# Optimization experiments

Measured on AMD Instinct MI355X. Metric: run time of the kernel, lower is better.

## Reference

```python
import jax, jax.numpy as jnp
import numpy as np

B, N, D, H = 1, 512, 128, 128  # batch, seq, pair dim, hidden dim
EPS = 1e-6  # flax nnx LayerNorm default epsilon


def _layernorm(x, scale, bias):
    m = jnp.mean(x, axis=-1, keepdims=True)
    v = jnp.var(x, axis=-1, keepdims=True)
    return (x - m) * jax.lax.rsqrt(v + EPS) * scale + bias


def setup_inputs() -> dict:
    key = jax.random.key(0)
    ks = jax.random.split(key, 12)
    s = 0.02  # param init scale
    inp = {
        "x": jax.random.normal(ks[0], (B, N, N, D), jnp.float32),
        "src_mask": jnp.ones((B, N), jnp.float32),
        # first LayerNorm
        "ln1_scale": jnp.ones((D,), jnp.float32),
        "ln1_bias": jnp.zeros((D,), jnp.float32),
        # left/right projections
        "wl": jax.random.normal(ks[1], (D, H), jnp.float32) * s,
        "bl": jnp.zeros((H,), jnp.float32),
        "wr": jax.random.normal(ks[2], (D, H), jnp.float32) * s,
        "br": jnp.zeros((H,), jnp.float32),
        # gates (original inits kernel=0, bias=1; use small random kernels + bias=1 for a nontrivial baseline)
        "wlg": jax.random.normal(ks[3], (D, H), jnp.float32) * s,
        "blg": jnp.ones((H,), jnp.float32),
        "wrg": jax.random.normal(ks[4], (D, H), jnp.float32) * s,
        "brg": jnp.ones((H,), jnp.float32),
        "wog": jax.random.normal(ks[5], (D, H), jnp.float32) * s,
        "bog": jnp.ones((H,), jnp.float32),
        # output LayerNorm + projection
        "ln2_scale": jnp.ones((H,), jnp.float32),
        "ln2_bias": jnp.zeros((H,), jnp.float32),
        "wo": jax.random.normal(ks[6], (H, D), jnp.float32) * s,
        "bo": jnp.zeros((D,), jnp.float32),
    }
    return inp


def reference(x, src_mask, ln1_scale, ln1_bias, wl, bl, wr, br, wlg, blg,
              wrg, brg, wog, bog, ln2_scale, ln2_bias, wo, bo):
    # mask[b,i,j] = src_mask[b,i] * src_mask[b,j]  -> [B,N,N,1]
    sm = src_mask.astype(jnp.float32)
    mask = (sm[:, :, None] * sm[:, None, :])[..., None]

    xn = _layernorm(x, ln1_scale, ln1_bias)  # [B,N,N,D]

    # projections, mask, gates (gating after transpose in the original is
    # elementwise, hence equivalent applied pre-transpose)
    left = (xn @ wl + bl) * mask * jax.nn.sigmoid(xn @ wlg + blg)   # [B,N,N,H]
    right = (xn @ wr + br) * mask * jax.nn.sigmoid(xn @ wrg + brg)  # [B,N,N,H]
    out_gate = jax.nn.sigmoid(xn @ wog + bog)                       # [B,N,N,H]

    # 'ingoing' mix: out[b,i,j,d] = sum_k left[b,k,i,d] * right[b,k,j,d]
    out = jnp.einsum('bkid,bkjd->bijd', left, right)

    out = _layernorm(out, ln2_scale, ln2_bias) * out_gate
    return out @ wo + bo
```

## Files before the change

### kernel.cpp

```cpp
#include <hip/hip_runtime.h>
#include <hip/hip_bf16.h>


#define NSEQ 512
#define NN 262144
#define DMODEL 128

typedef __attribute__((ext_vector_type(8))) short short8;
typedef __attribute__((ext_vector_type(4))) float f32x4;

__device__ __forceinline__ unsigned short f2b(float f) {
    __hip_bfloat16 h = __float2bfloat16(f);
    return *reinterpret_cast<unsigned short*>(&h);
}
__device__ __forceinline__ float b2f(unsigned short u) {
    __hip_bfloat16 h;
    *reinterpret_cast<unsigned short*>(&h) = u;
    return __bfloat162float(h);
}
__device__ __forceinline__ float sigmoidf_(float x) {
    return 1.0f / (1.0f + __expf(-x));
}

__global__ __launch_bounds__(256) void k_wt_all(
    const float* __restrict__ w0, const float* __restrict__ w1,
    const float* __restrict__ w2, const float* __restrict__ w3,
    const float* __restrict__ w4, const float* __restrict__ w5,
    unsigned short* __restrict__ wt) {
    int bid = blockIdx.x;
    int mat = bid >> 6;
    const float* w = (mat == 0) ? w0 : (mat == 1) ? w1 : (mat == 2) ? w2
                   : (mat == 3) ? w3 : (mat == 4) ? w4 : w5;
    int idx = (bid & 63) * 256 + threadIdx.x;
    int d = idx >> 7, h = idx & 127;
    wt[mat * 16384 + h * 128 + d] = f2b(w[idx]);
}

__global__ __launch_bounds__(256) void k_ln1(const float* __restrict__ x,
                                             const float* __restrict__ sc,
                                             const float* __restrict__ bi,
                                             unsigned short* __restrict__ xn) {
    int t = threadIdx.x;
    int l = t & 31;
    size_t row = (size_t)blockIdx.x * 8 + (t >> 5);
    float4 v = *(const float4*)(x + row * DMODEL + l * 4);
    float s  = v.x + v.y + v.z + v.w;
    float sq = v.x * v.x + v.y * v.y + v.z * v.z + v.w * v.w;
    #pragma unroll
    for (int m = 1; m < 32; m <<= 1) {
        s  += __shfl_xor(s, m);
        sq += __shfl_xor(sq, m);
    }
    float mean = s * (1.f / 128.f);
    float var  = sq * (1.f / 128.f) - mean * mean;
    float inv  = rsqrtf(var + 1e-6f);
    float4 scv = *(const float4*)(sc + l * 4);
    float4 biv = *(const float4*)(bi + l * 4);
    unsigned long long o = 0;
    o |= (unsigned long long)f2b((v.x - mean) * inv * scv.x + biv.x);
    o |= (unsigned long long)f2b((v.y - mean) * inv * scv.y + biv.y) << 16;
    o |= (unsigned long long)f2b((v.z - mean) * inv * scv.z + biv.z) << 32;
    o |= (unsigned long long)f2b((v.w - mean) * inv * scv.w + biv.w) << 48;
    *(unsigned long long*)(xn + row * DMODEL + l * 4) = o;
}

__global__ __launch_bounds__(256, 2) void k_proj(
    const unsigned short* __restrict__ xn,
    const float* __restrict__ src_mask,
    const unsigned short* __restrict__ wt,
    const float* __restrict__ bl,  const float* __restrict__ blg,
    const float* __restrict__ br,  const float* __restrict__ brg,
    const float* __restrict__ bog,
    unsigned short* __restrict__ left_t,
    unsigned short* __restrict__ right_t,
    unsigned short* __restrict__ og) {
    __shared__ __align__(16) unsigned short As[64 * 136];
    const int t = threadIdx.x;
    const int lane = t & 63;
    const int wv = t >> 6;
    const int a0 = blockIdx.x * 64;
    const int b  = blockIdx.y;
    const int n0 = wv * 32;

    short8 bfA[2][4], bfB[2][4];
    auto loadB = [&](short8 (&dst)[2][4], int mat) {
        const unsigned short* base = wt + mat * 16384 + (lane >> 4) * 8;
        #pragma unroll
        for (int nf = 0; nf < 2; ++nf)
            #pragma unroll
            for (int kc = 0; kc < 4; ++kc)
                dst[nf][kc] = *(const short8*)(
                    base + (n0 + nf * 16 + (lane & 15)) * 128 + kc * 32);
    };
    loadB(bfA, 0);
    loadB(bfB, 1);

    #pragma unroll
    for (int it = 0; it < 4; ++it) {
        int idx = it * 256 + t;
        int row = idx >> 4, c = idx & 15;
        *(short8*)(&As[row * 136 + c * 8]) =
            *(const short8*)(xn + ((size_t)(a0 + row) * NSEQ + b) * DMODEL + c * 8);
    }
    __syncthreads();

    short8 af[4][4];
    #pragma unroll
    for (int mf = 0; mf < 4; ++mf)
        #pragma unroll
        for (int kc = 0; kc < 4; ++kc)
            af[mf][kc] = *(const short8*)(
                &As[(mf * 16 + (lane & 15)) * 136 + kc * 32 + (lane >> 4) * 8]);

    f32x4 acc0[4][2], acc1[4][2];
    float smb = src_mask[b];

    auto mmat = [&](f32x4 (&acc)[4][2], short8 (&bf)[2][4]) {
        #pragma unroll
        for (int mf = 0; mf < 4; ++mf)
            #pragma unroll
            for (int nf = 0; nf < 2; ++nf)
                acc[mf][nf] = f32x4{0.f, 0.f, 0.f, 0.f};
        #pragma unroll
        for (int kc = 0; kc < 4; ++kc)
            #pragma unroll
            for (int mf = 0; mf < 4; ++mf)
                #pragma unroll
                for (int nf = 0; nf < 2; ++nf)
                    acc[mf][nf] = __builtin_amdgcn_mfma_f32_16x16x32_bf16(
                        af[mf][kc], bf[nf][kc], acc[mf][nf], 0, 0, 0);
    };
    auto epi_pair = [&](const float* b1, const float* b2, unsigned short* dst) {
        #pragma unroll
        for (int nf = 0; nf < 2; ++nf) {
            int h = n0 + nf * 16 + (lane & 15);
            float b1v = b1[h], b2v = b2[h];
            #pragma unroll
            for (int mf = 0; mf < 4; ++mf) {
                int abase = a0 + mf * 16 + ((lane >> 4) << 2);
                unsigned long long pv64 = 0;
                #pragma unroll
                for (int j = 0; j < 4; ++j) {
                    float pv = acc0[mf][nf][j] + b1v;
                    float gv = acc1[mf][nf][j] + b2v;
                    float mk = src_mask[abase + j] * smb;
                    unsigned long long q = f2b(pv * mk * sigmoidf_(gv));
                    pv64 |= q << (16 * j);
                }
                *(unsigned long long*)(dst + (size_t)h * NN + (size_t)b * NSEQ + abase) = pv64;
            }
        }
    };

    mmat(acc0, bfA);
    loadB(bfA, 2);
    mmat(acc1, bfB);
    loadB(bfB, 3);
    epi_pair(bl, blg, left_t);
    mmat(acc0, bfA);
    loadB(bfA, 4);
    mmat(acc1, bfB);
    epi_pair(br, brg, right_t);
    mmat(acc0, bfA);

    __syncthreads();
    #pragma unroll
    for (int nf = 0; nf < 2; ++nf) {
        int h = n0 + nf * 16 + (lane & 15);
        float bv = bog[h];
        #pragma unroll
        for (int mf = 0; mf < 4; ++mf) {
            int rloc = mf * 16 + ((lane >> 4) << 2);
            #pragma unroll
            for (int j = 0; j < 4; ++j)
                As[(rloc + j) * 136 + h] = f2b(sigmoidf_(acc0[mf][nf][j] + bv));
        }
    }
    __syncthreads();
    #pragma unroll
    for (int it = 0; it < 4; ++it) {
        int idx = it * 256 + t;
        int row = idx >> 4, c = idx & 15;
        *(short8*)(og + ((size_t)(a0 + row) * NSEQ + b) * DMODEL + c * 8) =
            *(const short8*)(&As[row * 136 + c * 8]);
    }
}

__global__ __launch_bounds__(256) void k_einsum(
    const unsigned short* __restrict__ lt,
    const unsigned short* __restrict__ rt,
    unsigned short* __restrict__ mid) {
    __shared__ __align__(16) unsigned short As[2][128 * 36];
    __shared__ __align__(16) unsigned short Bs[2][128 * 36];
    const int t = threadIdx.x, lane = t & 63, wv = t >> 6;
    const int bid = blockIdx.x;
    const int xcd = bid & 7, slot = bid >> 3;
    const int d = xcd * 16 + (slot >> 4);
    const int tile = slot & 15;
    const int i0 = (tile >> 2) * 128, j0 = (tile & 3) * 128;
    const int m0 = (wv >> 1) * 64, n0 = (wv & 1) * 64;
    const unsigned short* Ag = lt + (size_t)d * NN;
    const unsigned short* Bg = rt + (size_t)d * NN;

    const int row0 = t >> 2, sub0 = t & 3;
    const int row1 = (256 + t) >> 2, sub1 = t & 3;

    short8 ra[2], rb[2];
    auto loadTile = [&](int k0) {
        ra[0] = *(const short8*)(Ag + (size_t)(i0 + row0) * NSEQ + k0 + sub0 * 8);
        rb[0] = *(const short8*)(Bg + (size_t)(j0 + row0) * NSEQ + k0 + sub0 * 8);
        ra[1] = *(const short8*)(Ag + (size_t)(i0 + row1) * NSEQ + k0 + sub1 * 8);
        rb[1] = *(const short8*)(Bg + (size_t)(j0 + row1) * NSEQ + k0 + sub1 * 8);
    };
    auto writeTile = [&](int buf) {
        *(short8*)(&As[buf][row0 * 36 + sub0 * 8]) = ra[0];
        *(short8*)(&Bs[buf][row0 * 36 + sub0 * 8]) = rb[0];
        *(short8*)(&As[buf][row1 * 36 + sub1 * 8]) = ra[1];
        *(short8*)(&Bs[buf][row1 * 36 + sub1 * 8]) = rb[1];
    };

    f32x4 acc[4][4];
    #pragma unroll
    for (int mf = 0; mf < 4; ++mf)
        #pragma unroll
        for (int nf = 0; nf < 4; ++nf)
            acc[mf][nf] = f32x4{0.f, 0.f, 0.f, 0.f};

    loadTile(0);
    writeTile(0);
    int cur = 0;
    const int ko = (lane >> 4) * 8;
    for (int it = 0; it < 16; ++it) {
        __syncthreads();
        if (it < 15) loadTile((it + 1) * 32);
        short8 af[4], bf[4];
        #pragma unroll
        for (int mf = 0; mf < 4; ++mf)
            af[mf] = *(const short8*)(&As[cur][(m0 + mf * 16 + (lane & 15)) * 36 + ko]);
        #pragma unroll
        for (int nf = 0; nf < 4; ++nf)
            bf[nf] = *(const short8*)(&Bs[cur][(n0 + nf * 16 + (lane & 15)) * 36 + ko]);
        #pragma unroll
        for (int mf = 0; mf < 4; ++mf)
            #pragma unroll
            for (int nf = 0; nf < 4; ++nf)
                acc[mf][nf] = __builtin_amdgcn_mfma_f32_16x16x32_bf16(
                    af[mf], bf[nf], acc[mf][nf], 0, 0, 0);
        if (it < 15) writeTile(cur ^ 1);
        cur ^= 1;
    }
    unsigned short* out = mid + (size_t)d * NN;
    #pragma unroll
    for (int mf = 0; mf < 4; ++mf) {
        int rbase = i0 + m0 + mf * 16 + ((lane >> 4) << 2);
        #pragma unroll
        for (int nf = 0; nf < 4; ++nf) {
            int col = j0 + n0 + nf * 16 + (lane & 15);
            #pragma unroll
            for (int j = 0; j < 4; ++j)
                out[(size_t)(rbase + j) * NSEQ + col] = f2b(acc[mf][nf][j]);
        }
    }
}

__global__ __launch_bounds__(128) void k_ln2gate(
    const unsigned short* __restrict__ mid,
    const unsigned short* __restrict__ og,
    const float* __restrict__ sc, const float* __restrict__ bi,
    unsigned short* __restrict__ g) {
    __shared__ __align__(16) unsigned short lo[128 * 136];
    const int t = threadIdx.x;
    const size_t p0 = (size_t)blockIdx.x * 128;
    const size_t p = p0 + t;

    unsigned int vals[64];
    float s = 0.f, sq = 0.f;
    #pragma unroll
    for (int d2 = 0; d2 < 64; ++d2) {
        unsigned int a = mid[(size_t)(2 * d2)     * NN + p];
        unsigned int c = mid[(size_t)(2 * d2 + 1) * NN + p];
        vals[d2] = a | (c << 16);
        float fa = b2f((unsigned short)a), fc = b2f((unsigned short)c);
        s += fa + fc; sq += fa * fa + fc * fc;
    }
    float mean = s * (1.f / 128.f);
    float var  = sq * (1.f / 128.f) - mean * mean;
    float inv  = rsqrtf(var + 1e-6f);
    #pragma unroll
    for (int c = 0; c < 16; ++c) {
        short8 ov = *(const short8*)(og + p * DMODEL + c * 8);
        short8 r8;
        #pragma unroll
        for (int e = 0; e < 8; ++e) {
            int d = c * 8 + e;
            unsigned int w = vals[d >> 1];
            float v = b2f((unsigned short)((d & 1) ? (w >> 16) : (w & 0xffff)));
            float y = (v - mean) * inv * sc[d] + bi[d];
            r8[e] = (short)f2b(y * b2f((unsigned short)ov[e]));
        }
        *(short8*)(&lo[t * 136 + c * 8]) = r8;
    }
    __syncthreads();
    #pragma unroll
    for (int i = 0; i < 16; ++i) {
        int idx = i * 128 + t;
        int row = idx >> 4, ch = idx & 15;
        *(short8*)(g + (p0 + row) * DMODEL + ch * 8) =
            *(const short8*)(&lo[row * 136 + ch * 8]);
    }
}

__global__ __launch_bounds__(256) void k_out(
    const unsigned short* __restrict__ g,
    const unsigned short* __restrict__ wt_o,
    const float* __restrict__ bo,
    float* __restrict__ out) {
    __shared__ __align__(16) unsigned short As[64 * 136];
    __shared__ __align__(16) unsigned short Bs[128 * 136];
    const int t = threadIdx.x, lane = t & 63, wv = t >> 6;
    const size_t r0 = (size_t)blockIdx.x * 64;
    const int n0 = wv * 32;
    for (int it = 0; it < 4; ++it) {
        int idx = it * 256 + t;
        int row = idx >> 4, c = idx & 15;
        *(short8*)(&As[row * 136 + c * 8]) =
            *(const short8*)(g + (r0 + row) * DMODEL + c * 8);
    }
    for (int it = 0; it < 8; ++it) {
        int idx = it * 256 + t;
        int h = idx >> 4, c = idx & 15;
        *(short8*)(&Bs[h * 136 + c * 8]) = *(const short8*)(wt_o + h * 128 + c * 8);
    }
    __syncthreads();
    f32x4 acc[4][2];
    #pragma unroll
    for (int mf = 0; mf < 4; ++mf)
        #pragma unroll
        for (int nf = 0; nf < 2; ++nf)
            acc[mf][nf] = f32x4{0.f, 0.f, 0.f, 0.f};
    #pragma unroll
    for (int kc = 0; kc < 4; ++kc) {
        int ko = kc * 32 + (lane >> 4) * 8;
        short8 af[4], bf[2];
        #pragma unroll
        for (int mf = 0; mf < 4; ++mf)
            af[mf] = *(const short8*)(&As[(mf * 16 + (lane & 15)) * 136 + ko]);
        #pragma unroll
        for (int nf = 0; nf < 2; ++nf)
            bf[nf] = *(const short8*)(&Bs[(n0 + nf * 16 + (lane & 15)) * 136 + ko]);
        #pragma unroll
        for (int mf = 0; mf < 4; ++mf)
            #pragma unroll
            for (int nf = 0; nf < 2; ++nf)
                acc[mf][nf] = __builtin_amdgcn_mfma_f32_16x16x32_bf16(
                    af[mf], bf[nf], acc[mf][nf], 0, 0, 0);
    }
    #pragma unroll
    for (int nf = 0; nf < 2; ++nf) {
        int n = n0 + nf * 16 + (lane & 15);
        float bv = bo[n];
        #pragma unroll
        for (int mf = 0; mf < 4; ++mf) {
            int rb = mf * 16 + ((lane >> 4) << 2);
            #pragma unroll
            for (int j = 0; j < 4; ++j)
                out[(r0 + rb + j) * DMODEL + n] = acc[mf][nf][j] + bv;
        }
    }
}

extern "C" void kernel_launch(void* const* d_in, const int* in_sizes, int n_in,
                              void* d_out, int out_size, void* d_ws, size_t ws_size,
                              hipStream_t stream) {
    const float* x    = (const float*)d_in[0];
    const float* sm   = (const float*)d_in[1];
    const float* ln1s = (const float*)d_in[2];
    const float* ln1b = (const float*)d_in[3];
    const float* wl   = (const float*)d_in[4];
    const float* bl   = (const float*)d_in[5];
    const float* wr   = (const float*)d_in[6];
    const float* br   = (const float*)d_in[7];
    const float* wlg  = (const float*)d_in[8];
    const float* blg  = (const float*)d_in[9];
    const float* wrg  = (const float*)d_in[10];
    const float* brg  = (const float*)d_in[11];
    const float* wog  = (const float*)d_in[12];
    const float* bog  = (const float*)d_in[13];
    const float* ln2s = (const float*)d_in[14];
    const float* ln2b = (const float*)d_in[15];
    const float* wo   = (const float*)d_in[16];
    const float* bo   = (const float*)d_in[17];
    float* out = (float*)d_out;

    char* ws = (char*)d_ws;
    unsigned short* wt  = (unsigned short*)ws;
    unsigned short* xn  = (unsigned short*)(ws + 196608);
    unsigned short* lt  = (unsigned short*)(ws + 196608 + 1ull * 67108864);
    unsigned short* rt  = (unsigned short*)(ws + 196608 + 2ull * 67108864);
    unsigned short* ogb = (unsigned short*)(ws + 196608 + 3ull * 67108864);
    unsigned short* mid = (unsigned short*)(ws + 196608 + 4ull * 67108864);
    unsigned short* gb  = xn;

    k_wt_all<<<384, 256, 0, stream>>>(wl, wlg, wr, wrg, wog, wo, wt);
    k_ln1<<<32768, 256, 0, stream>>>(x, ln1s, ln1b, xn);
    k_proj<<<dim3(8, 512), 256, 0, stream>>>(xn, sm, wt,
                                             bl, blg, br, brg, bog, lt, rt, ogb);
    k_einsum<<<2048, 256, 0, stream>>>(lt, rt, mid);
    k_ln2gate<<<2048, 128, 0, stream>>>(mid, ogb, ln2s, ln2b, gb);
    k_out<<<4096, 256, 0, stream>>>(gb, wt + 5 * 16384, bo, out);
}
```

Measured before the change: 320.2 us.

## Pad per-channel plane stride, use packed bf16 converts and fast sigmoid

The per-channel planes for left, right and mid now use a padded stride (PL instead of NN), so consecutive channel planes no longer sit a power-of-two distance apart; this targets channel/bank conflicts in the einsum and the strided LN2 reads. Manual bf16 packing is replaced with the v_cvt_pk_bf16_f32 instruction, and the sigmoid uses exp2 plus rcp intrinsics. In k_proj the mask values are hoisted out of the inner loop and the occupancy hint rises from 2 to 4 blocks per SM. The workspace layout grows to hold the padded planes, and the fast sigmoid trades a little precision for fewer instructions.

```diff
diff --git a/kernel.cpp b/kernel.cpp
--- a/kernel.cpp
+++ b/kernel.cpp
@@ -4,6 +4,7 @@
 
 #define NSEQ 512
 #define NN 262144
+#define PL 262400
 #define DMODEL 128
 
 typedef __attribute__((ext_vector_type(8))) short short8;
@@ -18,8 +19,13 @@
     *reinterpret_cast<unsigned short*>(&h) = u;
     return __bfloat162float(h);
 }
-__device__ __forceinline__ float sigmoidf_(float x) {
-    return 1.0f / (1.0f + __expf(-x));
+__device__ __forceinline__ unsigned int cvt_pk_bf16(float lo, float hi) {
+    unsigned int r;
+    asm("v_cvt_pk_bf16_f32 %0, %1, %2" : "=v"(r) : "v"(lo), "v"(hi));
+    return r;
+}
+__device__ __forceinline__ float sigfast(float x) {
+    return __builtin_amdgcn_rcpf(1.f + __builtin_amdgcn_exp2f(x * -1.44269504f));
 }
 
 __global__ __launch_bounds__(256) void k_wt_all(
@@ -56,15 +62,15 @@
     float inv  = rsqrtf(var + 1e-6f);
     float4 scv = *(const float4*)(sc + l * 4);
     float4 biv = *(const float4*)(bi + l * 4);
-    unsigned long long o = 0;
-    o |= (unsigned long long)f2b((v.x - mean) * inv * scv.x + biv.x);
-    o |= (unsigned long long)f2b((v.y - mean) * inv * scv.y + biv.y) << 16;
-    o |= (unsigned long long)f2b((v.z - mean) * inv * scv.z + biv.z) << 32;
-    o |= (unsigned long long)f2b((v.w - mean) * inv * scv.w + biv.w) << 48;
-    *(unsigned long long*)(xn + row * DMODEL + l * 4) = o;
-}
-
-__global__ __launch_bounds__(256, 2) void k_proj(
+    uint2 pk;
+    pk.x = cvt_pk_bf16((v.x - mean) * inv * scv.x + biv.x,
+                       (v.y - mean) * inv * scv.y + biv.y);
+    pk.y = cvt_pk_bf16((v.z - mean) * inv * scv.z + biv.z,
+                       (v.w - mean) * inv * scv.w + biv.w);
+    *(uint2*)(xn + row * DMODEL + l * 4) = pk;
+}
+
+__global__ __launch_bounds__(256, 4) void k_proj(
     const unsigned short* __restrict__ xn,
     const float* __restrict__ src_mask,
     const unsigned short* __restrict__ wt,
@@ -131,6 +137,13 @@
                         af[mf][kc], bf[nf][kc], acc[mf][nf], 0, 0, 0);
     };
     auto epi_pair = [&](const float* b1, const float* b2, unsigned short* dst) {
+        float mkv[16];
+        #pragma unroll
+        for (int mf = 0; mf < 4; ++mf)
+            #pragma unroll
+            for (int j = 0; j < 4; ++j)
+                mkv[mf * 4 + j] =
+                    src_mask[a0 + mf * 16 + ((lane >> 4) << 2) + j] * smb;
         #pragma unroll
         for (int nf = 0; nf < 2; ++nf) {
             int h = n0 + nf * 16 + (lane & 15);
@@ -138,16 +151,17 @@
             #pragma unroll
             for (int mf = 0; mf < 4; ++mf) {
                 int abase = a0 + mf * 16 + ((lane >> 4) << 2);
-                unsigned long long pv64 = 0;
+                float o_[4];
                 #pragma unroll
                 for (int j = 0; j < 4; ++j) {
                     float pv = acc0[mf][nf][j] + b1v;
                     float gv = acc1[mf][nf][j] + b2v;
-                    float mk = src_mask[abase + j] * smb;
-                    unsigned long long q = f2b(pv * mk * sigmoidf_(gv));
-                    pv64 |= q << (16 * j);
+                    o_[j] = pv * mkv[mf * 4 + j] * sigfast(gv);
                 }
-                *(unsigned long long*)(dst + (size_t)h * NN + (size_t)b * NSEQ + abase) = pv64;
+                uint2 pk;
+                pk.x = cvt_pk_bf16(o_[0], o_[1]);
+                pk.y = cvt_pk_bf16(o_[2], o_[3]);
+                *(uint2*)(dst + (size_t)h * PL + (size_t)b * NSEQ + abase) = pk;
             }
         }
     };
@@ -173,7 +187,7 @@
             int rloc = mf * 16 + ((lane >> 4) << 2);
             #pragma unroll
             for (int j = 0; j < 4; ++j)
-                As[(rloc + j) * 136 + h] = f2b(sigmoidf_(acc0[mf][nf][j] + bv));
+                As[(rloc + j) * 136 + h] = f2b(sigfast(acc0[mf][nf][j] + bv));
         }
     }
     __syncthreads();
@@ -199,8 +213,8 @@
     const int tile = slot & 15;
     const int i0 = (tile >> 2) * 128, j0 = (tile & 3) * 128;
     const int m0 = (wv >> 1) * 64, n0 = (wv & 1) * 64;
-    const unsigned short* Ag = lt + (size_t)d * NN;
-    const unsigned short* Bg = rt + (size_t)d * NN;
+    const unsigned short* Ag = lt + (size_t)d * PL;
+    const unsigned short* Bg = rt + (size_t)d * PL;
 
     const int row0 = t >> 2, sub0 = t & 3;
     const int row1 = (256 + t) >> 2, sub1 = t & 3;
@@ -249,7 +263,7 @@
         if (it < 15) writeTile(cur ^ 1);
         cur ^= 1;
     }
-    unsigned short* out = mid + (size_t)d * NN;
+    unsigned short* out = mid + (size_t)d * PL;
     #pragma unroll
     for (int mf = 0; mf < 4; ++mf) {
         int rbase = i0 + m0 + mf * 16 + ((lane >> 4) << 2);
@@ -277,8 +291,8 @@
     float s = 0.f, sq = 0.f;
     #pragma unroll
     for (int d2 = 0; d2 < 64; ++d2) {
-        unsigned int a = mid[(size_t)(2 * d2)     * NN + p];
-        unsigned int c = mid[(size_t)(2 * d2 + 1) * NN + p];
+        unsigned int a = mid[(size_t)(2 * d2)     * PL + p];
+        unsigned int c = mid[(size_t)(2 * d2 + 1) * PL + p];
         vals[d2] = a | (c << 16);
         float fa = b2f((unsigned short)a), fc = b2f((unsigned short)c);
         s += fa + fc; sq += fa * fa + fc * fc;
@@ -289,16 +303,20 @@
     #pragma unroll
     for (int c = 0; c < 16; ++c) {
         short8 ov = *(const short8*)(og + p * DMODEL + c * 8);
-        short8 r8;
+        float y[8];
         #pragma unroll
         for (int e = 0; e < 8; ++e) {
             int d = c * 8 + e;
             unsigned int w = vals[d >> 1];
             float v = b2f((unsigned short)((d & 1) ? (w >> 16) : (w & 0xffff)));
-            float y = (v - mean) * inv * sc[d] + bi[d];
-            r8[e] = (short)f2b(y * b2f((unsigned short)ov[e]));
+            y[e] = ((v - mean) * inv * sc[d] + bi[d]) * b2f((unsigned short)ov[e]);
         }
-        *(short8*)(&lo[t * 136 + c * 8]) = r8;
+        uint4 pk;
+        pk.x = cvt_pk_bf16(y[0], y[1]);
+        pk.y = cvt_pk_bf16(y[2], y[3]);
+        pk.z = cvt_pk_bf16(y[4], y[5]);
+        pk.w = cvt_pk_bf16(y[6], y[7]);
+        *(uint4*)(&lo[t * 136 + c * 8]) = pk;
     }
     __syncthreads();
     #pragma unroll
@@ -393,12 +411,14 @@
     float* out = (float*)d_out;
 
     char* ws = (char*)d_ws;
+    const size_t SZ_XN = 67108864ull;
+    const size_t SZ_PL = (size_t)PL * 128 * 2;
     unsigned short* wt  = (unsigned short*)ws;
     unsigned short* xn  = (unsigned short*)(ws + 196608);
-    unsigned short* lt  = (unsigned short*)(ws + 196608 + 1ull * 67108864);
-    unsigned short* rt  = (unsigned short*)(ws + 196608 + 2ull * 67108864);
-    unsigned short* ogb = (unsigned short*)(ws + 196608 + 3ull * 67108864);
-    unsigned short* mid = (unsigned short*)(ws + 196608 + 4ull * 67108864);
+    unsigned short* lt  = (unsigned short*)(ws + 196608 + SZ_XN);
+    unsigned short* rt  = (unsigned short*)(ws + 196608 + SZ_XN + SZ_PL);
+    unsigned short* ogb = (unsigned short*)(ws + 196608 + SZ_XN + 2 * SZ_PL);
+    unsigned short* mid = (unsigned short*)(ws + 196608 + 2 * SZ_XN + 2 * SZ_PL);
     unsigned short* gb  = xn;
 
     k_wt_all<<<384, 256, 0, stream>>>(wl, wlg, wr, wrg, wog, wo, wt);
```

After: 639.8 us. 99.8% more time.
